# Kernel optimization log

Measured on AMD Instinct MI355X. Metric: run time of the kernel, lower is better.

Reference implementation:

```python
import jax, jax.numpy as jnp
import numpy as np

B, S = 512, 200            # batch, max_seq_len
D = H = 512                # embedding_dim must equal hidden_dim (ht init from embedded input)
VOCAB, USERS, SKILLS, OUT = 2002, 10000, 1001, 1001


def setup_inputs() -> dict:
    key = jax.random.key(0)
    ks = jax.random.split(key, 15)
    s = 0.05
    enc_emb = jax.random.normal(ks[0], (VOCAB, D)) * s
    enc_emb = enc_emb.at[0].set(0.0)  # padding_idx=0
    P = jax.random.normal(ks[1], (USERS, H)) * s
    Q = jax.random.normal(ks[2], (SKILLS, H)) * s
    P_bias = jax.random.normal(ks[3], (USERS, 1)) * s
    Q_bias = jax.random.normal(ks[4], (SKILLS, 1)) * s
    W_ih = jax.random.normal(ks[5], (4 * H, D)) * s   # torch LSTMCell weight_ih
    W_hh = jax.random.normal(ks[6], (4 * H, H)) * s   # torch LSTMCell weight_hh
    b_ih = jax.random.normal(ks[7], (4 * H,)) * s
    b_hh = jax.random.normal(ks[8], (4 * H,)) * s
    dec_W = jax.random.normal(ks[9], (OUT, H)) * s    # nn.Linear weight
    dec_b = jax.random.normal(ks[10], (OUT,)) * s
    main_input = jax.random.randint(ks[11], (B, S), 0, VOCAB)
    target_id = jax.random.randint(ks[12], (B, 1), 0, OUT)
    user_id_sequence = jax.random.randint(ks[13], (B, S), 0, USERS)
    skill_id_sequence = jax.random.randint(ks[14], (B, S), 0, SKILLS)
    return dict(main_input=main_input, target_id=target_id,
                user_id_sequence=user_id_sequence, skill_id_sequence=skill_id_sequence,
                enc_emb=enc_emb, P=P, Q=Q, P_bias=P_bias, Q_bias=Q_bias,
                W_ih=W_ih, W_hh=W_hh, b_ih=b_ih, b_hh=b_hh, dec_W=dec_W, dec_b=dec_b)


def reference(main_input, target_id, user_id_sequence, skill_id_sequence,
              enc_emb, P, Q, P_bias, Q_bias, W_ih, W_hh, b_ih, b_hh, dec_W, dec_b):
    x = enc_emb[main_input]                                    # [B,S,D] (dropout in eval mode = identity)
    # MF extended input: sigmoid(sum(P*Q, dim=2, keepdim) + P_bias + Q_bias) -> [B,S,1]
    mf = jax.nn.sigmoid(jnp.sum(P[user_id_sequence] * Q[skill_id_sequence], axis=2, keepdims=True)
                        + P_bias[user_id_sequence] + Q_bias[skill_id_sequence])

    def step(carry, inp):
        ht, ct = carry
        xt, et = inp                                           # xt:[B,D], et:[B,1]
        ct = ct + ct * et                                      # custom gating before cell update
        gates = xt @ W_ih.T + b_ih + ht @ W_hh.T + b_hh        # [B,4H], torch gate order i,f,g,o
        i, f, g, o = jnp.split(gates, 4, axis=-1)
        ct = jax.nn.sigmoid(f) * ct + jax.nn.sigmoid(i) * jnp.tanh(g)
        ht = jax.nn.sigmoid(o) * jnp.tanh(ct)
        return (ht, ct), None

    h0 = jnp.zeros((x.shape[0], H), x.dtype)
    (ht, _), _ = jax.lax.scan(step, (h0, h0),
                              (jnp.swapaxes(x, 0, 1), jnp.swapaxes(mf, 0, 1)))
    out = ht @ dec_W.T + dec_b                                 # [B,OUT]
    out = jnp.take_along_axis(out, target_id, axis=-1)         # [B,1]
    return jax.nn.sigmoid(out)
```

## Files before the change

kernel.cpp:

```cpp
#include <hip/hip_runtime.h>

typedef __attribute__((ext_vector_type(8))) short short8;
typedef __attribute__((ext_vector_type(4))) float floatx4;
typedef unsigned int uint;
typedef unsigned short ushort;
typedef unsigned long long ull;
typedef __attribute__((ext_vector_type(4))) uint uintx4;
typedef __attribute__((ext_vector_type(4))) int intx4;

#define B_ 512
#define S_ 200
#define H_ 512
#define VOCAB_ 2002

__device__ __forceinline__ ushort f2bfbits(float f) {
  union { float f; uint u; } c; c.f = f;
  uint u = c.u;
  u += 0x7fffu + ((u >> 16) & 1u);
  return (ushort)(u >> 16);
}
__device__ __forceinline__ float bf2f_(ushort u) {
  union { uint i; float f; } c; c.i = ((uint)u) << 16; return c.f;
}
__device__ __forceinline__ float sigmoidf_(float x) { return 1.f / (1.f + __expf(-x)); }
__device__ __forceinline__ float tanhf_(float x) { return 2.f / (1.f + __expf(-2.f * x)) - 1.f; }
__device__ __forceinline__ float clamp30(float x) { return fminf(fmaxf(x, -30.f), 30.f); }

__device__ __forceinline__ void split8(const float* p, short8& hi, short8& lo) {
#pragma unroll
  for (int j = 0; j < 8; ++j) {
    const float f = p[j];
    const ushort h = f2bfbits(f);
    hi[j] = (short)h;
    lo[j] = (short)f2bfbits(f - bf2f_(h));
  }
}

__device__ __forceinline__ void ld32_cc(const void* p, uintx4& a, uintx4& b) {
  asm volatile("global_load_dwordx4 %0, %2, off sc0 sc1\n\t"
               "global_load_dwordx4 %1, %2, off offset:16 sc0 sc1"
               : "=&v"(a), "=&v"(b)
               : "v"(p));
}
__device__ __forceinline__ void ld32_cc_wait(const void* p, intx4& a, intx4& b) {
  asm volatile("global_load_dwordx4 %0, %2, off sc0 sc1\n\t"
               "global_load_dwordx4 %1, %2, off offset:16 sc0 sc1\n\t"
               "s_waitcnt vmcnt(0)"
               : "=&v"(a), "=&v"(b)
               : "v"(p)
               : "memory");
}
__device__ __forceinline__ void vm_wait0() {
  asm volatile("s_waitcnt vmcnt(0)" ::: "memory");
}

template <typename ET>
__global__ void encg_kernel(const float* __restrict__ emb, const float* __restrict__ Wih,
                            ET* __restrict__ encg) {
  const int w = threadIdx.x >> 6, l = threadIdx.x & 63;
  const int ln = l & 15, lk = l >> 4;
  const int n = (blockIdx.x * 4 + w) * 16 + ln;
  const int m = blockIdx.y * 16 + ln;
  const int mA = (m < VOCAB_) ? m : 0;
  const float* ap = emb + (size_t)mA * 512 + lk * 8;
  const float* bp = Wih + (size_t)n * 512 + lk * 8;
  floatx4 acc = {0.f, 0.f, 0.f, 0.f};
#pragma unroll 4
  for (int kk = 0; kk < 16; ++kk) {
    short8 ah, al, bh, bl;
    split8(ap + kk * 32, ah, al);
    split8(bp + kk * 32, bh, bl);
    acc = __builtin_amdgcn_mfma_f32_16x16x32_bf16(ah, bh, acc, 0, 0, 0);
    acc = __builtin_amdgcn_mfma_f32_16x16x32_bf16(ah, bl, acc, 0, 0, 0);
    acc = __builtin_amdgcn_mfma_f32_16x16x32_bf16(al, bh, acc, 0, 0, 0);
  }
#pragma unroll
  for (int r = 0; r < 4; ++r) {
    const int mo = blockIdx.y * 16 + lk * 4 + r;
    if (mo < VOCAB_) {
      if constexpr (sizeof(ET) == 2)
        encg[(size_t)mo * 2048 + n] = (ET)f2bfbits(acc[r]);
      else
        encg[(size_t)mo * 2048 + n] = acc[r];
    }
  }
}

__global__ void mf_kernel(const int* __restrict__ us, const int* __restrict__ ss,
                          const float* __restrict__ P, const float* __restrict__ Q,
                          const float* __restrict__ Pb, const float* __restrict__ Qb,
                          float* __restrict__ etb) {
  const int s = blockIdx.x;
  const int w = threadIdx.x >> 6, l = threadIdx.x & 63;
  const int b = blockIdx.y * 4 + w;
  const int u = us[b * S_ + s];
  const int k = ss[b * S_ + s];
  const float4 p0 = *(const float4*)(P + (size_t)u * 512 + l * 8);
  const float4 p1 = *(const float4*)(P + (size_t)u * 512 + l * 8 + 4);
  const float4 q0 = *(const float4*)(Q + (size_t)k * 512 + l * 8);
  const float4 q1 = *(const float4*)(Q + (size_t)k * 512 + l * 8 + 4);
  float dot = p0.x*q0.x + p0.y*q0.y + p0.z*q0.z + p0.w*q0.w
            + p1.x*q1.x + p1.y*q1.y + p1.z*q1.z + p1.w*q1.w;
#pragma unroll
  for (int off = 32; off > 0; off >>= 1) dot += __shfl_xor(dot, off);
  if (l == 0)
    etb[s * B_ + b] = sigmoidf_(dot + Pb[u] + Qb[k]);
}

template <typename ET>
__global__ __launch_bounds__(512, 2) void lstm_kernel(
    const int* __restrict__ tok, const ET* __restrict__ encg,
    const float* __restrict__ etb, const float* __restrict__ Whh,
    const float* __restrict__ bih, const float* __restrict__ bhh,
    ushort* ht_hi, ushort* ht_lo, int* ctr) {
  __shared__ __align__(16) ushort Ah_lds[32 * 512];
  __shared__ __align__(16) ushort Al_lds[32 * 512];
  __shared__ float gp_lds[128 * 37];

  const int bid = blockIdx.x;
  const int g = bid & 15, ns = bid >> 4;
  const int b0 = g * 32, h0 = ns * 32;
  const int tid = threadIdx.x;
  const int w = tid >> 6, l = tid & 63;
  const int ln = l & 15, lk = l >> 4;
  const int q = w >> 1;
  const int c0w = (w & 1) * 16;

  int* const myslot = ctr + g * 256 + ns * 16;
  const int* const gslots = ctr + g * 256;

  short8 Bh[16], Bl[16];
  {
    const float* wr = Whh + (size_t)(q * 512 + h0 + c0w + ln) * 512 + lk * 8;
#pragma unroll 4
    for (int kk = 0; kk < 16; ++kk)
      split8(wr + kk * 32, Bh[kk], Bl[kk]);
  }

  const int sr = tid >> 4;
  const int sc = tid & 15;
  const int hh = sc * 2;
  const int bg = b0 + sr;
  float ct0 = 0.f, ct1 = 0.f;

  float bs[4][2];
#pragma unroll
  for (int qq = 0; qq < 4; ++qq) {
    const int col = qq * 512 + h0 + hh;
    bs[qq][0] = bih[col] + bhh[col];
    bs[qq][1] = bih[col + 1] + bhh[col + 1];
  }

  const int swzw = (sr & 7) << 3;
  const int swzr = (ln & 7) << 3;

  for (int s = 0; s < S_; ++s) {
    const int tv = tok[bg * S_ + s];
    float ev = etb[s * B_ + bg];
    float ex[4], ey[4];
#pragma unroll
    for (int qq = 0; qq < 4; ++qq) {
      if constexpr (sizeof(ET) == 2) {
        const uint e2 = *(const uint*)((const ushort*)encg + (size_t)tv * 2048 + qq * 512 + h0 + hh);
        ex[qq] = bf2f_((ushort)(e2 & 0xffffu)); ey[qq] = bf2f_((ushort)(e2 >> 16));
      } else {
        const float2 e = *(const float2*)((const float*)encg + (size_t)tv * 2048 + qq * 512 + h0 + hh);
        ex[qq] = e.x; ey[qq] = e.y;
      }
    }

    if (s > 0 && tid < 16) {
      const int* sp = gslots + tid * 16;
      for (;;) {
        intx4 va, vb;
        ld32_cc_wait(sp, va, vb);
        if (va[0] >= s && va[1] >= s && va[2] >= s && va[3] >= s &&
            vb[0] >= s && vb[1] >= s && vb[2] >= s && vb[3] >= s) break;
      }
    }
    __syncthreads();

    const size_t rdo = (size_t)(s & 1) * (B_ * H_);
    const size_t wro = (size_t)((s & 1) ^ 1) * (B_ * H_);
    const ushort* hrow = ht_hi + rdo + (size_t)bg * 512;
    const ushort* lrow = ht_lo + rdo + (size_t)bg * 512;

    {
      const int c = sc * 16;
      uintx4 ah0, ah1, al0, al1;
      ld32_cc(hrow + c, ah0, ah1);
      ld32_cc(lrow + c, al0, al1);
      vm_wait0();
      const int d0 = sr * 512 + (c ^ swzw);
      const int d1 = sr * 512 + ((c + 8) ^ swzw);
      *(uintx4*)(Ah_lds + d0) = ah0; *(uintx4*)(Ah_lds + d1) = ah1;
      *(uintx4*)(Al_lds + d0) = al0; *(uintx4*)(Al_lds + d1) = al1;
    }
    __syncthreads();

    const int c1 = 256 + sc * 16;
    uintx4 nh0, nh1, nl0, nl1;
    ld32_cc(hrow + c1, nh0, nh1);
    ld32_cc(lrow + c1, nl0, nl1);

    floatx4 acc0 = {0.f, 0.f, 0.f, 0.f};
    floatx4 acc1 = {0.f, 0.f, 0.f, 0.f};
#pragma unroll
    for (int kk = 0; kk < 8; ++kk) {
      const int csw = (kk * 32 + lk * 8) ^ swzr;
      {
        const int ao = ln * 512 + csw;
        const short8 ah = *(const short8*)(Ah_lds + ao);
        const short8 al = *(const short8*)(Al_lds + ao);
        acc0 = __builtin_amdgcn_mfma_f32_16x16x32_bf16(ah, Bh[kk], acc0, 0, 0, 0);
        acc0 = __builtin_amdgcn_mfma_f32_16x16x32_bf16(ah, Bl[kk], acc0, 0, 0, 0);
        acc0 = __builtin_amdgcn_mfma_f32_16x16x32_bf16(al, Bh[kk], acc0, 0, 0, 0);
      }
      {
        const int ao = (16 + ln) * 512 + csw;
        const short8 ah = *(const short8*)(Ah_lds + ao);
        const short8 al = *(const short8*)(Al_lds + ao);
        acc1 = __builtin_amdgcn_mfma_f32_16x16x32_bf16(ah, Bh[kk], acc1, 0, 0, 0);
        acc1 = __builtin_amdgcn_mfma_f32_16x16x32_bf16(ah, Bl[kk], acc1, 0, 0, 0);
        acc1 = __builtin_amdgcn_mfma_f32_16x16x32_bf16(al, Bh[kk], acc1, 0, 0, 0);
      }
    }

    vm_wait0();
    __builtin_amdgcn_sched_barrier(0);
    {
      const int d0 = sr * 512 + (c1 ^ swzw);
      const int d1 = sr * 512 + ((c1 + 8) ^ swzw);
      *(uintx4*)(Ah_lds + d0) = nh0; *(uintx4*)(Ah_lds + d1) = nh1;
      *(uintx4*)(Al_lds + d0) = nl0; *(uintx4*)(Al_lds + d1) = nl1;
    }
    __syncthreads();

#pragma unroll
    for (int kk = 8; kk < 16; ++kk) {
      const int csw = (kk * 32 + lk * 8) ^ swzr;
      {
        const int ao = ln * 512 + csw;
        const short8 ah = *(const short8*)(Ah_lds + ao);
        const short8 al = *(const short8*)(Al_lds + ao);
        acc0 = __builtin_amdgcn_mfma_f32_16x16x32_bf16(ah, Bh[kk], acc0, 0, 0, 0);
        acc0 = __builtin_amdgcn_mfma_f32_16x16x32_bf16(ah, Bl[kk], acc0, 0, 0, 0);
        acc0 = __builtin_amdgcn_mfma_f32_16x16x32_bf16(al, Bh[kk], acc0, 0, 0, 0);
      }
      {
        const int ao = (16 + ln) * 512 + csw;
        const short8 ah = *(const short8*)(Ah_lds + ao);
        const short8 al = *(const short8*)(Al_lds + ao);
        acc1 = __builtin_amdgcn_mfma_f32_16x16x32_bf16(ah, Bh[kk], acc1, 0, 0, 0);
        acc1 = __builtin_amdgcn_mfma_f32_16x16x32_bf16(ah, Bl[kk], acc1, 0, 0, 0);
        acc1 = __builtin_amdgcn_mfma_f32_16x16x32_bf16(al, Bh[kk], acc1, 0, 0, 0);
      }
    }

    {
      const int gb = (w * 16 + ln) * 37;
#pragma unroll
      for (int r = 0; r < 4; ++r) {
        gp_lds[gb + lk * 4 + r] = acc0[r];
        gp_lds[gb + 16 + lk * 4 + r] = acc1[r];
      }
    }
    __syncthreads();

    {
      ev = fminf(fmaxf(ev, 0.f), 1.f);
      float Gv[4][2];
#pragma unroll
      for (int qq = 0; qq < 4; ++qq) {
        Gv[qq][0] = clamp30(gp_lds[(qq * 32 + hh) * 37 + sr] + ex[qq] + bs[qq][0]);
        Gv[qq][1] = clamp30(gp_lds[(qq * 32 + hh + 1) * 37 + sr] + ey[qq] + bs[qq][1]);
      }
      const float scale = 1.f + ev;
      float c0v = ct0 * scale;
      c0v = sigmoidf_(Gv[1][0]) * c0v + sigmoidf_(Gv[0][0]) * tanhf_(Gv[2][0]);
      const float h0v = sigmoidf_(Gv[3][0]) * tanhf_(c0v);
      ct0 = c0v;
      float c1v = ct1 * scale;
      c1v = sigmoidf_(Gv[1][1]) * c1v + sigmoidf_(Gv[0][1]) * tanhf_(Gv[2][1]);
      const float h1v = sigmoidf_(Gv[3][1]) * tanhf_(c1v);
      ct1 = c1v;
      const ushort h0h = f2bfbits(h0v), h1h = f2bfbits(h1v);
      const ushort h0l = f2bfbits(h0v - bf2f_(h0h)), h1l = f2bfbits(h1v - bf2f_(h1h));
      const size_t wo = wro + (size_t)bg * 512 + h0 + hh;
      __hip_atomic_store((uint*)(ht_hi + wo), (uint)h0h | ((uint)h1h << 16),
                         __ATOMIC_RELAXED, __HIP_MEMORY_SCOPE_AGENT);
      __hip_atomic_store((uint*)(ht_lo + wo), (uint)h0l | ((uint)h1l << 16),
                         __ATOMIC_RELAXED, __HIP_MEMORY_SCOPE_AGENT);
    }

    vm_wait0();
    if (l == 0)
      __hip_atomic_store(myslot + w, s + 1, __ATOMIC_RELAXED, __HIP_MEMORY_SCOPE_AGENT);
  }
}

__global__ void dec_kernel(const ushort* __restrict__ hthi, const ushort* __restrict__ htlo,
                           const float* __restrict__ decW, const float* __restrict__ decb,
                           const int* __restrict__ tgt, float* __restrict__ out) {
  const int w = threadIdx.x >> 6, l = threadIdx.x & 63;
  const int b = blockIdx.x * 4 + w;
  const int t = tgt[b];
  const uint4 hv = *(const uint4*)(hthi + (size_t)b * 512 + l * 8);
  const uint4 lv = *(const uint4*)(htlo + (size_t)b * 512 + l * 8);
  const float4 w0 = *(const float4*)(decW + (size_t)t * 512 + l * 8);
  const float4 w1 = *(const float4*)(decW + (size_t)t * 512 + l * 8 + 4);
  const uint ha[4] = {hv.x, hv.y, hv.z, hv.w};
  const uint la[4] = {lv.x, lv.y, lv.z, lv.w};
  float hf[8];
#pragma unroll
  for (int i = 0; i < 4; ++i) {
    hf[2*i]   = bf2f_((ushort)(ha[i] & 0xffffu)) + bf2f_((ushort)(la[i] & 0xffffu));
    hf[2*i+1] = bf2f_((ushort)(ha[i] >> 16))     + bf2f_((ushort)(la[i] >> 16));
  }
  float dot = hf[0]*w0.x + hf[1]*w0.y + hf[2]*w0.z + hf[3]*w0.w
            + hf[4]*w1.x + hf[5]*w1.y + hf[6]*w1.z + hf[7]*w1.w;
#pragma unroll
  for (int off = 32; off > 0; off >>= 1) dot += __shfl_xor(dot, off);
  if (l == 0) out[b] = sigmoidf_(dot + decb[t]);
}

extern "C" void kernel_launch(void* const* d_in, const int* in_sizes, int n_in,
                              void* d_out, int out_size, void* d_ws, size_t ws_size,
                              hipStream_t stream) {
  (void)in_sizes; (void)n_in; (void)out_size;
  const int* main_input = (const int*)d_in[0];
  const int* target_id  = (const int*)d_in[1];
  const int* user_seq   = (const int*)d_in[2];
  const int* skill_seq  = (const int*)d_in[3];
  const float* enc_emb  = (const float*)d_in[4];
  const float* P        = (const float*)d_in[5];
  const float* Q        = (const float*)d_in[6];
  const float* Pb       = (const float*)d_in[7];
  const float* Qb       = (const float*)d_in[8];
  const float* W_ih     = (const float*)d_in[9];
  const float* W_hh     = (const float*)d_in[10];
  const float* b_ih     = (const float*)d_in[11];
  const float* b_hh     = (const float*)d_in[12];
  const float* dec_W    = (const float*)d_in[13];
  const float* dec_b    = (const float*)d_in[14];
  float* out = (float*)d_out;

  char* wsb = (char*)d_ws;
  ushort* ht_hi = (ushort*)wsb;
  ushort* ht_lo = (ushort*)(wsb + 1048576);
  int* ctr = (int*)(wsb + 2097152);
  float* etb = (float*)(wsb + 2113536);
  char* encb = wsb + 2523136;
  const bool enc32 = ws_size >= (size_t)2523136 + 16400384;

  hipMemsetAsync(wsb, 0, 2113536, stream);

  if (enc32)
    encg_kernel<float><<<dim3(32, 126), dim3(256), 0, stream>>>(enc_emb, W_ih, (float*)encb);
  else
    encg_kernel<ushort><<<dim3(32, 126), dim3(256), 0, stream>>>(enc_emb, W_ih, (ushort*)encb);
  mf_kernel<<<dim3(200, 128), dim3(256), 0, stream>>>(user_seq, skill_seq, P, Q, Pb, Qb, etb);
  if (enc32)
    lstm_kernel<float><<<dim3(256), dim3(512), 0, stream>>>(
        main_input, (const float*)encb, etb, W_hh, b_ih, b_hh, ht_hi, ht_lo, ctr);
  else
    lstm_kernel<ushort><<<dim3(256), dim3(512), 0, stream>>>(
        main_input, (const ushort*)encb, etb, W_hh, b_ih, b_hh, ht_hi, ht_lo, ctr);
  dec_kernel<<<dim3(128), dim3(256), 0, stream>>>(ht_hi, ht_lo, dec_W, dec_b, target_id, out);
}
```

Before: 2.871 ms.

## Switch recurrent GEMM to 32x32 MFMA with split-K across wave halves

Replaces the 16x16x32 MFMA tiling with 32x32x16 MFMA tiles, where each wave owns one gate's 32 columns and half of the K dimension. Both h halves are loaded up front. The first K-half waves compute while the second half of h is staged into LDS, then the second K-half waves compute. The two partial sums are reduced in the pointwise stage through a doubled gp_lds buffer. It also adds s_sleep to the inter-block spin wait. The aim is fewer MFMA instructions and LDS reads per step, traded against serialising the two K halves across wave groups, which may leave half the waves idle during each phase.

Measured after the change: 2.879 ms. About the same (+0.3%).

```diff
diff --git a/kernel.cpp b/kernel.cpp
--- a/kernel.cpp
+++ b/kernel.cpp
@@ -2,6 +2,7 @@
 
 typedef __attribute__((ext_vector_type(8))) short short8;
 typedef __attribute__((ext_vector_type(4))) float floatx4;
+typedef __attribute__((ext_vector_type(16))) float floatx16;
 typedef unsigned int uint;
 typedef unsigned short ushort;
 typedef unsigned long long ull;
@@ -52,6 +53,9 @@
 }
 __device__ __forceinline__ void vm_wait0() {
   asm volatile("s_waitcnt vmcnt(0)" ::: "memory");
+}
+__device__ __forceinline__ void vm_wait4() {
+  asm volatile("s_waitcnt vmcnt(4)" ::: "memory");
 }
 
 template <typename ET>
@@ -115,26 +119,26 @@
     ushort* ht_hi, ushort* ht_lo, int* ctr) {
   __shared__ __align__(16) ushort Ah_lds[32 * 512];
   __shared__ __align__(16) ushort Al_lds[32 * 512];
-  __shared__ float gp_lds[128 * 37];
+  __shared__ float gp_lds[2 * 128 * 33];
 
   const int bid = blockIdx.x;
   const int g = bid & 15, ns = bid >> 4;
   const int b0 = g * 32, h0 = ns * 32;
   const int tid = threadIdx.x;
   const int w = tid >> 6, l = tid & 63;
-  const int ln = l & 15, lk = l >> 4;
-  const int q = w >> 1;
-  const int c0w = (w & 1) * 16;
+  const int nt = w & 3;
+  const int kh = w >> 2;
 
   int* const myslot = ctr + g * 256 + ns * 16;
   const int* const gslots = ctr + g * 256;
 
   short8 Bh[16], Bl[16];
   {
-    const float* wr = Whh + (size_t)(q * 512 + h0 + c0w + ln) * 512 + lk * 8;
+    const float* wr = Whh + (size_t)(nt * 512 + h0 + (l & 31)) * 512
+                    + kh * 256 + (l >> 5) * 8;
 #pragma unroll 4
     for (int kk = 0; kk < 16; ++kk)
-      split8(wr + kk * 32, Bh[kk], Bl[kk]);
+      split8(wr + kk * 16, Bh[kk], Bl[kk]);
   }
 
   const int sr = tid >> 4;
@@ -152,7 +156,30 @@
   }
 
   const int swzw = (sr & 7) << 3;
-  const int swzr = (ln & 7) << 3;
+  const int swzr = (l & 7) << 3;
+  const int khbase = kh * 256;
+  const int k8 = (l >> 5) * 8;
+
+  auto mfma_half = [&](int base) -> floatx16 {
+    floatx16 a = {0.f,0.f,0.f,0.f,0.f,0.f,0.f,0.f,
+                  0.f,0.f,0.f,0.f,0.f,0.f,0.f,0.f};
+#pragma unroll
+    for (int kk = 0; kk < 16; ++kk) {
+      const int ao = (l & 31) * 512 + ((base + kk * 16 + k8) ^ swzr);
+      const short8 ah = *(const short8*)(Ah_lds + ao);
+      const short8 al = *(const short8*)(Al_lds + ao);
+      a = __builtin_amdgcn_mfma_f32_32x32x16_bf16(ah, Bh[kk], a, 0, 0, 0);
+      a = __builtin_amdgcn_mfma_f32_32x32x16_bf16(ah, Bl[kk], a, 0, 0, 0);
+      a = __builtin_amdgcn_mfma_f32_32x32x16_bf16(al, Bh[kk], a, 0, 0, 0);
+    }
+    return a;
+  };
+  auto gp_write = [&](const floatx16& a) {
+    float* gpw = gp_lds + kh * 4224 + (nt * 32 + (l & 31)) * 33 + 4 * (l >> 5);
+#pragma unroll
+    for (int r = 0; r < 16; ++r)
+      gpw[(r & 3) + 8 * (r >> 2)] = a[r];
+  };
 
   for (int s = 0; s < S_; ++s) {
     const int tv = tok[bg * S_ + s];
@@ -176,6 +203,7 @@
         ld32_cc_wait(sp, va, vb);
         if (va[0] >= s && va[1] >= s && va[2] >= s && va[3] >= s &&
             vb[0] >= s && vb[1] >= s && vb[2] >= s && vb[3] >= s) break;
+        __builtin_amdgcn_s_sleep(2);
       }
     }
     __syncthreads();
@@ -185,85 +213,47 @@
     const ushort* hrow = ht_hi + rdo + (size_t)bg * 512;
     const ushort* lrow = ht_lo + rdo + (size_t)bg * 512;
 
-    {
-      const int c = sc * 16;
-      uintx4 ah0, ah1, al0, al1;
-      ld32_cc(hrow + c, ah0, ah1);
-      ld32_cc(lrow + c, al0, al1);
-      vm_wait0();
-      const int d0 = sr * 512 + (c ^ swzw);
-      const int d1 = sr * 512 + ((c + 8) ^ swzw);
-      *(uintx4*)(Ah_lds + d0) = ah0; *(uintx4*)(Ah_lds + d1) = ah1;
-      *(uintx4*)(Al_lds + d0) = al0; *(uintx4*)(Al_lds + d1) = al1;
-    }
-    __syncthreads();
-
-    const int c1 = 256 + sc * 16;
+    const int c0 = sc * 16, c1 = 256 + sc * 16;
+    uintx4 h00, h01, l00, l01;
     uintx4 nh0, nh1, nl0, nl1;
+    __builtin_amdgcn_sched_barrier(0);
+    ld32_cc(hrow + c0, h00, h01);
+    ld32_cc(lrow + c0, l00, l01);
     ld32_cc(hrow + c1, nh0, nh1);
     ld32_cc(lrow + c1, nl0, nl1);
-
-    floatx4 acc0 = {0.f, 0.f, 0.f, 0.f};
-    floatx4 acc1 = {0.f, 0.f, 0.f, 0.f};
-#pragma unroll
-    for (int kk = 0; kk < 8; ++kk) {
-      const int csw = (kk * 32 + lk * 8) ^ swzr;
-      {
-        const int ao = ln * 512 + csw;
-        const short8 ah = *(const short8*)(Ah_lds + ao);
-        const short8 al = *(const short8*)(Al_lds + ao);
-        acc0 = __builtin_amdgcn_mfma_f32_16x16x32_bf16(ah, Bh[kk], acc0, 0, 0, 0);
-        acc0 = __builtin_amdgcn_mfma_f32_16x16x32_bf16(ah, Bl[kk], acc0, 0, 0, 0);
-        acc0 = __builtin_amdgcn_mfma_f32_16x16x32_bf16(al, Bh[kk], acc0, 0, 0, 0);
-      }
-      {
-        const int ao = (16 + ln) * 512 + csw;
-        const short8 ah = *(const short8*)(Ah_lds + ao);
-        const short8 al = *(const short8*)(Al_lds + ao);
-        acc1 = __builtin_amdgcn_mfma_f32_16x16x32_bf16(ah, Bh[kk], acc1, 0, 0, 0);
-        acc1 = __builtin_amdgcn_mfma_f32_16x16x32_bf16(ah, Bl[kk], acc1, 0, 0, 0);
-        acc1 = __builtin_amdgcn_mfma_f32_16x16x32_bf16(al, Bh[kk], acc1, 0, 0, 0);
-      }
-    }
-
-    vm_wait0();
+    vm_wait4();
     __builtin_amdgcn_sched_barrier(0);
     {
-      const int d0 = sr * 512 + (c1 ^ swzw);
-      const int d1 = sr * 512 + ((c1 + 8) ^ swzw);
-      *(uintx4*)(Ah_lds + d0) = nh0; *(uintx4*)(Ah_lds + d1) = nh1;
-      *(uintx4*)(Al_lds + d0) = nl0; *(uintx4*)(Al_lds + d1) = nl1;
+      const int d0 = sr * 512 + (c0 ^ swzw);
+      const int d1 = sr * 512 + ((c0 + 8) ^ swzw);
+      *(uintx4*)(Ah_lds + d0) = h00; *(uintx4*)(Ah_lds + d1) = h01;
+      *(uintx4*)(Al_lds + d0) = l00; *(uintx4*)(Al_lds + d1) = l01;
     }
     __syncthreads();
 
-#pragma unroll
-    for (int kk = 8; kk < 16; ++kk) {
-      const int csw = (kk * 32 + lk * 8) ^ swzr;
-      {
-        const int ao = ln * 512 + csw;
-        const short8 ah = *(const short8*)(Ah_lds + ao);
-        const short8 al = *(const short8*)(Al_lds + ao);
-        acc0 = __builtin_amdgcn_mfma_f32_16x16x32_bf16(ah, Bh[kk], acc0, 0, 0, 0);
-        acc0 = __builtin_amdgcn_mfma_f32_16x16x32_bf16(ah, Bl[kk], acc0, 0, 0, 0);
-        acc0 = __builtin_amdgcn_mfma_f32_16x16x32_bf16(al, Bh[kk], acc0, 0, 0, 0);
-      }
-      {
-        const int ao = (16 + ln) * 512 + csw;
-        const short8 ah = *(const short8*)(Ah_lds + ao);
-        const short8 al = *(const short8*)(Al_lds + ao);
-        acc1 = __builtin_amdgcn_mfma_f32_16x16x32_bf16(ah, Bh[kk], acc1, 0, 0, 0);
-        acc1 = __builtin_amdgcn_mfma_f32_16x16x32_bf16(ah, Bl[kk], acc1, 0, 0, 0);
-        acc1 = __builtin_amdgcn_mfma_f32_16x16x32_bf16(al, Bh[kk], acc1, 0, 0, 0);
-      }
-    }
-
-    {
-      const int gb = (w * 16 + ln) * 37;
-#pragma unroll
-      for (int r = 0; r < 4; ++r) {
-        gp_lds[gb + lk * 4 + r] = acc0[r];
-        gp_lds[gb + 16 + lk * 4 + r] = acc1[r];
-      }
+    floatx16 acc;
+    if (kh == 0) {
+      acc = mfma_half(0);
+      gp_write(acc);
+      vm_wait0();
+      __builtin_amdgcn_sched_barrier(0);
+      const int e0 = sr * 512 + (c1 ^ swzw);
+      const int e1 = sr * 512 + ((c1 + 8) ^ swzw);
+      *(uintx4*)(Ah_lds + e0) = nh0; *(uintx4*)(Ah_lds + e1) = nh1;
+      *(uintx4*)(Al_lds + e0) = nl0; *(uintx4*)(Al_lds + e1) = nl1;
+    } else {
+      vm_wait0();
+      __builtin_amdgcn_sched_barrier(0);
+      const int e0 = sr * 512 + (c1 ^ swzw);
+      const int e1 = sr * 512 + ((c1 + 8) ^ swzw);
+      *(uintx4*)(Ah_lds + e0) = nh0; *(uintx4*)(Ah_lds + e1) = nh1;
+      *(uintx4*)(Al_lds + e0) = nl0; *(uintx4*)(Al_lds + e1) = nl1;
+    }
+    __syncthreads();
+
+    if (kh == 1) {
+      acc = mfma_half(256);
+      gp_write(acc);
     }
     __syncthreads();
 
@@ -272,8 +262,10 @@
       float Gv[4][2];
 #pragma unroll
       for (int qq = 0; qq < 4; ++qq) {
-        Gv[qq][0] = clamp30(gp_lds[(qq * 32 + hh) * 37 + sr] + ex[qq] + bs[qq][0]);
-        Gv[qq][1] = clamp30(gp_lds[(qq * 32 + hh + 1) * 37 + sr] + ey[qq] + bs[qq][1]);
+        const int cb0 = (qq * 32 + hh) * 33 + sr;
+        const int cb1 = (qq * 32 + hh + 1) * 33 + sr;
+        Gv[qq][0] = clamp30(gp_lds[cb0] + gp_lds[4224 + cb0] + ex[qq] + bs[qq][0]);
+        Gv[qq][1] = clamp30(gp_lds[cb1] + gp_lds[4224 + cb1] + ey[qq] + bs[qq][1]);
       }
       const float scale = 1.f + ev;
       float c0v = ct0 * scale;
```
